# Kernel optimization log

Measured on AMD Instinct MI355X. Metric: run time of the kernel, lower is better.

The kernel has to match this reference:

```python
import jax, jax.numpy as jnp
import numpy as np

# Module config (mirrors init_kwargs)
VMIN, VMAX = -1.0, 1.0
NUM_ACT_WEIGHTS = 31
INIT_SCALE = 0.04
FEATURES_OUT = 64
N, C, H, W = 8, 64, 256, 256


def setup_inputs() -> dict:
    key = jax.random.key(0)
    x = jax.random.normal(key, (N, C, H, W), dtype=jnp.float32)
    # mu: kernel centers, linspace over [vmin, vmax]
    mu = jnp.asarray(np.linspace(VMIN, VMAX, NUM_ACT_WEIGHTS, dtype=np.float32))
    # sigma: scalar std
    sigma = jnp.float32(2.0 * VMAX / (NUM_ACT_WEIGHTS - 1))
    # w: init_type 'linear' -> init_scale * x_0, repeated over feature channels
    w0 = (INIT_SCALE * np.linspace(VMIN, VMAX, NUM_ACT_WEIGHTS, dtype=np.float32))
    w0 = np.reshape(w0, (1, 1, 1, 1, NUM_ACT_WEIGHTS))
    w = jnp.asarray(np.repeat(w0, FEATURES_OUT, axis=1))  # (1,C,1,1,K)
    return {"x": x, "w": w, "mu": mu, "sigma": sigma}


def reference(x, w, mu, sigma):
    # output = sum_i w[...,i] * exp(-(x - mu_i)^2 / (2 sigma^2))
    inv_two_sig2 = 1.0 / (2.0 * sigma * sigma)
    K = w.shape[-1]
    out = jnp.zeros_like(x)
    # K is small and fixed (31); loop keeps peak memory at one NxCxHxW temp
    for i in range(K):
        d = x - mu[i]
        out = out + w[:, :, :, :, i] * jnp.exp(-(d * d) * inv_two_sig2)
    return out
```

## Files before the change

kernel.cpp:

```cpp
#include <hip/hip_runtime.h>


static constexpr int KW    = 31;
static constexpr int WIN   = 9;
static constexpr int RAD   = 4;
static constexpr int LUT_N = 1024;

typedef float f32x4 __attribute__((ext_vector_type(4)));
typedef float f32x2 __attribute__((ext_vector_type(2)));

__device__ __forceinline__ float rbf_win(float xe, const float* __restrict__ wrow,
                                         float mu0, float inv_d, float cd2, float g) {
    const float t = (xe - mu0) * inv_d;
    float jf = rintf(t) - (float)RAD;
    jf = fminf(fmaxf(jf, 0.0f), (float)(KW - WIN));
    const int s = (int)jf;
    float n = t - jf;
    n = fminf(fmaxf(n, -32.0f), 40.0f);
    float E = __builtin_amdgcn_exp2f(cd2 * n * n);
    float r = __builtin_amdgcn_exp2f(cd2 * fmaf(-2.0f, n, 1.0f));
    float acc = 0.0f;
#pragma unroll
    for (int k = 0; k < WIN; ++k) {
        acc = fmaf(wrow[s + k], E, acc);
        E *= r;
        r *= g;
    }
    return acc;
}

__device__ __forceinline__ void lut_setup(const float* __restrict__ w,
                                          const float* __restrict__ mu,
                                          const float* __restrict__ sigma,
                                          int c, int tid,
                                          float* lutA, float* wrow,
                                          float& invh, float& nlo, float& tmax) {
    const float mu0   = mu[0];
    const float muL   = mu[KW - 1];
    const float dmu   = (muL - mu0) * (1.0f / (KW - 1));
    const float inv_d = 1.0f / dmu;
    const float sg    = sigma[0];
    const float cd2   = -1.4426950408889634f * dmu * dmu / (2.0f * sg * sg);
    const float g     = exp2f(2.0f * cd2);

    const float pad  = 5.25f * sg;
    const float lo   = mu0 - pad;
    const float span = (muL - mu0) + 2.0f * pad;
    const float h    = span * (1.0f / (float)LUT_N);
    invh = (float)LUT_N / span;
    nlo  = -lo * invh;
    tmax = (float)LUT_N - 0.001f;

    if (tid < KW) wrow[tid] = w[c * KW + tid];
    __syncthreads();

    for (int e = tid; e <= LUT_N; e += 256)
        lutA[e] = rbf_win(lo + (float)e * h, wrow, mu0, inv_d, cd2, g);
    __syncthreads();
}

__device__ __forceinline__ float lut_eval(float xe, const float* __restrict__ lutA,
                                          float invh, float nlo, float tmax) {
    float t = fmaf(xe, invh, nlo);
    t = fminf(fmaxf(t, 0.0f), tmax);
    const int j = (int)t;
    const float frac = t - (float)j;
    const float a = lutA[j];
    const float b = lutA[j + 1];
    return fmaf(frac, b - a, a);
}

__global__ __launch_bounds__(256) void rbf_lut_fixed(
    const float* __restrict__ x, const float* __restrict__ w,
    const float* __restrict__ mu, const float* __restrict__ sigma,
    float* __restrict__ out) {
    __shared__ float lutA[LUT_N + 2];
    __shared__ float wrow[32];

    const int tid = threadIdx.x;
    const int c   = blockIdx.x >> 5;
    const int s   = blockIdx.x & 31;
    const int n   = s >> 2;
    const int q   = s & 3;

    int i4 = ((n << 6) + c) * 16384 + (q << 12) + tid;
    f32x4 xv = reinterpret_cast<const f32x4*>(x)[i4];

    float invh, nlo, tmax;
    lut_setup(w, mu, sigma, c, tid, lutA, wrow, invh, nlo, tmax);

#pragma unroll
    for (int k = 0; k < 16; ++k) {
        f32x4 xn;
        if (k < 15) xn = reinterpret_cast<const f32x4*>(x)[i4 + 256];
        f32x4 ov;
        ov.x = lut_eval(xv.x, lutA, invh, nlo, tmax);
        ov.y = lut_eval(xv.y, lutA, invh, nlo, tmax);
        ov.z = lut_eval(xv.z, lutA, invh, nlo, tmax);
        ov.w = lut_eval(xv.w, lutA, invh, nlo, tmax);
        __builtin_nontemporal_store(ov, reinterpret_cast<f32x4*>(out) + i4);
        xv = xn;
        i4 += 256;
    }
}

__global__ __launch_bounds__(256) void rbf_lut_generic(
    const float* __restrict__ x, const float* __restrict__ w,
    const float* __restrict__ mu, const float* __restrict__ sigma,
    float* __restrict__ out, int n4, int ntot, int iters, int c_shift) {
    __shared__ float lutA[LUT_N + 2];
    __shared__ float wrow[32];

    const int tid = threadIdx.x;
    const int gs  = gridDim.x * blockDim.x;
    const int gid = blockIdx.x * blockDim.x + tid;
    const int c   = (gid >> c_shift) & 63;

    float invh, nlo, tmax;
    lut_setup(w, mu, sigma, c, tid, lutA, wrow, invh, nlo, tmax);

    int i4 = gid;
    for (int k = 0; k < iters; ++k) {
        if (i4 < n4) {
            const f32x4 xv = reinterpret_cast<const f32x4*>(x)[i4];
            f32x4 ov;
            ov.x = lut_eval(xv.x, lutA, invh, nlo, tmax);
            ov.y = lut_eval(xv.y, lutA, invh, nlo, tmax);
            ov.z = lut_eval(xv.z, lutA, invh, nlo, tmax);
            ov.w = lut_eval(xv.w, lutA, invh, nlo, tmax);
            __builtin_nontemporal_store(ov, reinterpret_cast<f32x4*>(out) + i4);
        }
        i4 += gs;
    }

    const float mu0 = mu[0];
    const float dmu = (mu[KW - 1] - mu0) * (1.0f / (KW - 1));
    const float sg  = sigma[0];
    const float cd2x = -1.4426950408889634f / (2.0f * sg * sg);
    for (int i = n4 * 4 + gid; i < ntot; i += gs) {
        const float xe = x[i];
        const int ct = (i >> (c_shift + 2)) & 63;
        float acc = 0.0f;
        for (int qq = 0; qq < KW; ++qq) {
            const float d = xe - (mu0 + (float)qq * dmu);
            acc = fmaf(w[ct * KW + qq], __builtin_amdgcn_exp2f(cd2x * d * d), acc);
        }
        out[i] = acc;
    }
}

extern "C" void kernel_launch(void* const* d_in, const int* in_sizes, int n_in,
                              void* d_out, int out_size, void* d_ws, size_t ws_size,
                              hipStream_t stream) {
    const float* x  = (const float*)d_in[0];
    const float* w  = (const float*)d_in[1];
    const float* mu = (const float*)d_in[2];
    const float* sg = (const float*)d_in[3];
    float* out = (float*)d_out;

    if (out_size == 8 * 64 * 65536) {
        rbf_lut_fixed<<<2048, 256, 0, stream>>>(x, w, mu, sg, out);
    } else {
        const int n4     = out_size >> 2;
        const int blocks = 4096;
        const int gsz    = blocks * 256;
        const int iters  = (n4 + gsz - 1) / gsz;
        rbf_lut_generic<<<blocks, 256, 0, stream>>>(x, w, mu, sg, out, n4, out_size,
                                                    iters, 14);
    }
}
```

Before: 45.77 us.

## Store LUT as value/slope pairs and remap blocks across batch stride

```diff
diff --git a/kernel.cpp b/kernel.cpp
--- a/kernel.cpp
+++ b/kernel.cpp
@@ -33,7 +33,7 @@
                                           const float* __restrict__ mu,
                                           const float* __restrict__ sigma,
                                           int c, int tid,
-                                          float* lutA, float* wrow,
+                                          f32x2* lutP, float* vals, float* wrow,
                                           float& invh, float& nlo, float& tmax) {
     const float mu0   = mu[0];
     const float muL   = mu[KW - 1];
@@ -55,52 +55,56 @@
     __syncthreads();
 
     for (int e = tid; e <= LUT_N; e += 256)
-        lutA[e] = rbf_win(lo + (float)e * h, wrow, mu0, inv_d, cd2, g);
+        vals[e] = rbf_win(lo + (float)e * h, wrow, mu0, inv_d, cd2, g);
+    __syncthreads();
+
+    for (int e = tid; e < LUT_N; e += 256) {
+        f32x2 p; p.x = vals[e]; p.y = vals[e + 1] - vals[e];
+        lutP[e] = p;
+    }
     __syncthreads();
 }
 
-__device__ __forceinline__ float lut_eval(float xe, const float* __restrict__ lutA,
+__device__ __forceinline__ float lut_eval(float xe, const f32x2* __restrict__ lutP,
                                           float invh, float nlo, float tmax) {
     float t = fmaf(xe, invh, nlo);
     t = fminf(fmaxf(t, 0.0f), tmax);
     const int j = (int)t;
     const float frac = t - (float)j;
-    const float a = lutA[j];
-    const float b = lutA[j + 1];
-    return fmaf(frac, b - a, a);
+    const f32x2 ab = lutP[j];
+    return fmaf(frac, ab.y, ab.x);
 }
 
 __global__ __launch_bounds__(256) void rbf_lut_fixed(
     const float* __restrict__ x, const float* __restrict__ w,
     const float* __restrict__ mu, const float* __restrict__ sigma,
     float* __restrict__ out) {
-    __shared__ float lutA[LUT_N + 2];
+    __shared__ f32x2 lutP[LUT_N];
+    __shared__ float vals[LUT_N + 1];
     __shared__ float wrow[32];
 
     const int tid = threadIdx.x;
-    const int c   = blockIdx.x >> 5;
-    const int s   = blockIdx.x & 31;
-    const int n   = s >> 2;
-    const int q   = s & 3;
+    const int gid = blockIdx.x * 256 + tid;
+    const int c   = (gid >> 14) & 63;
 
-    int i4 = ((n << 6) + c) * 16384 + (q << 12) + tid;
+    int i4 = gid;
     f32x4 xv = reinterpret_cast<const f32x4*>(x)[i4];
 
     float invh, nlo, tmax;
-    lut_setup(w, mu, sigma, c, tid, lutA, wrow, invh, nlo, tmax);
+    lut_setup(w, mu, sigma, c, tid, lutP, vals, wrow, invh, nlo, tmax);
 
 #pragma unroll
-    for (int k = 0; k < 16; ++k) {
+    for (int k = 0; k < 8; ++k) {
         f32x4 xn;
-        if (k < 15) xn = reinterpret_cast<const f32x4*>(x)[i4 + 256];
+        if (k < 7) xn = reinterpret_cast<const f32x4*>(x)[i4 + (1 << 20)];
         f32x4 ov;
-        ov.x = lut_eval(xv.x, lutA, invh, nlo, tmax);
-        ov.y = lut_eval(xv.y, lutA, invh, nlo, tmax);
-        ov.z = lut_eval(xv.z, lutA, invh, nlo, tmax);
-        ov.w = lut_eval(xv.w, lutA, invh, nlo, tmax);
+        ov.x = lut_eval(xv.x, lutP, invh, nlo, tmax);
+        ov.y = lut_eval(xv.y, lutP, invh, nlo, tmax);
+        ov.z = lut_eval(xv.z, lutP, invh, nlo, tmax);
+        ov.w = lut_eval(xv.w, lutP, invh, nlo, tmax);
         __builtin_nontemporal_store(ov, reinterpret_cast<f32x4*>(out) + i4);
         xv = xn;
-        i4 += 256;
+        i4 += (1 << 20);
     }
 }
 
@@ -108,7 +112,8 @@
     const float* __restrict__ x, const float* __restrict__ w,
     const float* __restrict__ mu, const float* __restrict__ sigma,
     float* __restrict__ out, int n4, int ntot, int iters, int c_shift) {
-    __shared__ float lutA[LUT_N + 2];
+    __shared__ f32x2 lutP[LUT_N];
+    __shared__ float vals[LUT_N + 1];
     __shared__ float wrow[32];
 
     const int tid = threadIdx.x;
@@ -117,17 +122,17 @@
     const int c   = (gid >> c_shift) & 63;
 
     float invh, nlo, tmax;
-    lut_setup(w, mu, sigma, c, tid, lutA, wrow, invh, nlo, tmax);
+    lut_setup(w, mu, sigma, c, tid, lutP, vals, wrow, invh, nlo, tmax);
 
     int i4 = gid;
     for (int k = 0; k < iters; ++k) {
         if (i4 < n4) {
             const f32x4 xv = reinterpret_cast<const f32x4*>(x)[i4];
             f32x4 ov;
-            ov.x = lut_eval(xv.x, lutA, invh, nlo, tmax);
-            ov.y = lut_eval(xv.y, lutA, invh, nlo, tmax);
-            ov.z = lut_eval(xv.z, lutA, invh, nlo, tmax);
-            ov.w = lut_eval(xv.w, lutA, invh, nlo, tmax);
+            ov.x = lut_eval(xv.x, lutP, invh, nlo, tmax);
+            ov.y = lut_eval(xv.y, lutP, invh, nlo, tmax);
+            ov.z = lut_eval(xv.z, lutP, invh, nlo, tmax);
+            ov.w = lut_eval(xv.w, lutP, invh, nlo, tmax);
             __builtin_nontemporal_store(ov, reinterpret_cast<f32x4*>(out) + i4);
         }
         i4 += gs;
@@ -159,7 +164,7 @@
     float* out = (float*)d_out;
 
     if (out_size == 8 * 64 * 65536) {
-        rbf_lut_fixed<<<2048, 256, 0, stream>>>(x, w, mu, sg, out);
+        rbf_lut_fixed<<<4096, 256, 0, stream>>>(x, w, mu, sg, out);
     } else {
         const int n4     = out_size >> 2;
         const int blocks = 4096;
```

New measurement: 45.72 us. No clear change (-0.1%).
